# Kernel optimization log

Measured on AMD Instinct MI355X. Metric: run time of the kernel, lower is better.

Reference implementation:

```python
import jax, jax.numpy as jnp
import numpy as np

DIM_CODES = 512
DICT_SIZE = 512
EMBED_DIM = 16
BATCH = 512


def setup_inputs() -> dict:
    key = jax.random.key(0)
    k1, k2 = jax.random.split(key)
    mu = jax.random.normal(k1, (BATCH, DIM_CODES * EMBED_DIM), dtype=jnp.float32)
    dictionary = jax.random.normal(k2, (DIM_CODES, DICT_SIZE, EMBED_DIM), dtype=jnp.float32)
    return {"mu": mu, "dictionary": dictionary}


def reference(mu, dictionary):
    # mu: [B, C*E], dictionary: [C, K, E]
    B = mu.shape[0]
    C, K, E = dictionary.shape
    mu3 = mu.reshape(B, C, E)
    # pairwise squared distance ||mu - d||^2 = ||mu||^2 + ||d||^2 - 2 mu.d -> [B, C, K]
    dist = (jnp.sum(mu3 * mu3, axis=-1)[..., None]
            + jnp.sum(dictionary * dictionary, axis=-1)[None]
            - 2.0 * jnp.einsum('bce,cke->bck', mu3, dictionary))
    idx = jnp.argmin(dist, axis=-1)  # [B, C] int
    # gather nearest codebook entries: per-code index into its own codebook
    z_embed = dictionary[jnp.arange(C)[None, :], idx]  # [B, C, E]
    z_embed = z_embed.reshape(B, C * E)
    # TransferGrad: forward = z_embed, backward passes grad straight-through to mu
    z = mu + jax.lax.stop_gradient(z_embed - mu)
    one_hot_idx = jax.nn.one_hot(idx, K, dtype=mu.dtype)  # [B, C, K]
    return z, z_embed, one_hot_idx
```

## Files before the change

### kernel.cpp

```cpp
#include <hip/hip_runtime.h>
#include <float.h>

constexpr int C    = 512;
constexpr int K    = 512;
constexpr int E    = 16;
constexpr int B    = 512;
constexpr int ROWS = 128;
constexpr int MUS  = C * E;

__launch_bounds__(256, 2)
__global__ void vq_kernel(const float* __restrict__ mu,
                          const float* __restrict__ dict,
                          float* __restrict__ z,
                          float* __restrict__ zq,
                          float* __restrict__ oh)
{
    const int c    = blockIdx.x;
    const int b0   = blockIdx.y * ROWS;
    const int tid  = threadIdx.x;
    const int lane = tid & 63;
    const int wave = tid >> 6;

    __shared__ float mu_s[ROWS][E];

    const float* __restrict__ dbase = dict + (size_t)c * K * E;

    float4 dv[8][4];
    float  nrm[8];
#pragma unroll
    for (int i = 0; i < 8; ++i) {
        const int k = lane + 64 * i;
        const float4* p = reinterpret_cast<const float4*>(dbase + k * E);
        dv[i][0] = p[0]; dv[i][1] = p[1]; dv[i][2] = p[2]; dv[i][3] = p[3];
        float s = dv[i][0].x * dv[i][0].x;
        s = fmaf(dv[i][0].y, dv[i][0].y, s);
        s = fmaf(dv[i][0].z, dv[i][0].z, s);
        s = fmaf(dv[i][0].w, dv[i][0].w, s);
#pragma unroll
        for (int t = 1; t < 4; ++t) {
            s = fmaf(dv[i][t].x, dv[i][t].x, s);
            s = fmaf(dv[i][t].y, dv[i][t].y, s);
            s = fmaf(dv[i][t].z, dv[i][t].z, s);
            s = fmaf(dv[i][t].w, dv[i][t].w, s);
        }
        nrm[i] = s;
    }

    {
        const int r = tid >> 2, q = tid & 3;
#pragma unroll
        for (int rep = 0; rep < 2; ++rep) {
            const int row = r + rep * 64;
            const float4* p = reinterpret_cast<const float4*>(
                mu + (size_t)(b0 + row) * MUS + c * E);
            reinterpret_cast<float4*>(&mu_s[row][0])[q] = p[q];
        }
    }
    __syncthreads();

    auto compute_row = [&](int bl, float& obd, float& osec, int& obk) {
        float4 m[4];
#pragma unroll
        for (int t = 0; t < 4; ++t)
            m[t] = reinterpret_cast<const float4*>(&mu_s[bl][0])[t];

        float nm = m[0].x * m[0].x;
        nm = fmaf(m[0].y, m[0].y, nm);
        nm = fmaf(m[0].z, m[0].z, nm);
        nm = fmaf(m[0].w, m[0].w, nm);
#pragma unroll
        for (int t = 1; t < 4; ++t) {
            nm = fmaf(m[t].x, m[t].x, nm);
            nm = fmaf(m[t].y, m[t].y, nm);
            nm = fmaf(m[t].z, m[t].z, nm);
            nm = fmaf(m[t].w, m[t].w, nm);
        }

        float bdl = FLT_MAX, secl = FLT_MAX;
        int   bkl = K;
#pragma unroll
        for (int i = 0; i < 8; ++i) {
            float acc = dv[i][0].x * m[0].x;
            acc = fmaf(dv[i][0].y, m[0].y, acc);
            acc = fmaf(dv[i][0].z, m[0].z, acc);
            acc = fmaf(dv[i][0].w, m[0].w, acc);
#pragma unroll
            for (int t = 1; t < 4; ++t) {
                acc = fmaf(dv[i][t].x, m[t].x, acc);
                acc = fmaf(dv[i][t].y, m[t].y, acc);
                acc = fmaf(dv[i][t].z, m[t].z, acc);
                acc = fmaf(dv[i][t].w, m[t].w, acc);
            }
            const float dist = fmaf(-2.0f, acc, nm + nrm[i]);
            const int   k    = lane + 64 * i;
            const bool  lt   = dist < bdl;
            secl = lt ? bdl : fminf(secl, dist);
            bdl  = lt ? dist : bdl;
            bkl  = lt ? k : bkl;
        }
        obd = bdl; osec = secl; obk = bkl;
    };

    auto emit_row = [&](int bl_, float bd, float sec, int bk) {
        const int b = b0 + bl_;

        float w = bd;
#pragma unroll
        for (int off = 32; off; off >>= 1)
            w = fminf(w, __shfl_xor(w, off));

        const unsigned long long mask = __ballot(bd == w);
        const int lane0 = __ffsll(mask) - 1;
        int best_k = __shfl(bk, lane0);

        const float cand = (lane == lane0) ? sec : bd;
        if (__any(cand < w + 1e-3f)) {
            float mf[E];
#pragma unroll
            for (int t = 0; t < E; ++t) mf[t] = mu_s[bl_][t];
            double nmuD = 0.0;
#pragma unroll
            for (int t = 0; t < E; ++t) nmuD += (double)mf[t] * mf[t];

            double bD = DBL_MAX;
            int    bK = K;
#pragma unroll
            for (int i = 0; i < 8; ++i) {
                double nd = 0.0, dt = 0.0;
#pragma unroll
                for (int t = 0; t < 4; ++t) {
                    nd += (double)dv[i][t].x * dv[i][t].x
                        + (double)dv[i][t].y * dv[i][t].y
                        + (double)dv[i][t].z * dv[i][t].z
                        + (double)dv[i][t].w * dv[i][t].w;
                    dt += (double)dv[i][t].x * mf[4 * t + 0]
                        + (double)dv[i][t].y * mf[4 * t + 1]
                        + (double)dv[i][t].z * mf[4 * t + 2]
                        + (double)dv[i][t].w * mf[4 * t + 3];
                }
                const double dist = nmuD + nd - 2.0 * dt;
                const int k = lane + 64 * i;
                if (dist < bD) { bD = dist; bK = k; }
            }
#pragma unroll
            for (int off = 32; off; off >>= 1) {
                const double od = __shfl_down(bD, off);
                const int    ok = __shfl_down(bK, off);
                if (od < bD || (od == bD && ok < bK)) { bD = od; bK = ok; }
            }
            best_k = __shfl(bK, 0);
        }

        float* ohp = oh + ((size_t)b * C + c) * K;
#pragma unroll
        for (int h = 0; h < 2; ++h) {
            const int kb = h * 256 + lane * 4;
            float4 v;
            v.x = (kb + 0 == best_k) ? 1.0f : 0.0f;
            v.y = (kb + 1 == best_k) ? 1.0f : 0.0f;
            v.z = (kb + 2 == best_k) ? 1.0f : 0.0f;
            v.w = (kb + 3 == best_k) ? 1.0f : 0.0f;
            *reinterpret_cast<float4*>(ohp + kb) = v;
        }

        if (lane < E) {
            const float dq = dbase[best_k * E + lane];
            const float mm = mu_s[bl_][lane];
            const size_t o = (size_t)b * MUS + (size_t)c * E + lane;
            zq[o] = dq;
            z[o]  = mm + (dq - mm);
        }
    };

    {
        int   pbl = wave;
        float pbd, psec;
        int   pbk;
        compute_row(pbl, pbd, psec, pbk);

        for (int j = 1; j < ROWS / 4; ++j) {
            const int cbl = wave + 4 * j;
            float cbd, csec;
            int   cbk;
            compute_row(cbl, cbd, csec, cbk);
            emit_row(pbl, pbd, psec, pbk);
            pbl = cbl; pbd = cbd; psec = csec; pbk = cbk;
        }
        emit_row(pbl, pbd, psec, pbk);
    }
}

extern "C" void kernel_launch(void* const* d_in, const int* in_sizes, int n_in,
                              void* d_out, int out_size, void* d_ws, size_t ws_size,
                              hipStream_t stream)
{
    const float* mu   = (const float*)d_in[0];
    const float* dict = (const float*)d_in[1];

    float* z  = (float*)d_out;
    float* zq = z  + (size_t)B * C * E;
    float* oh = zq + (size_t)B * C * E;

    dim3 grid(C, B / ROWS);
    vq_kernel<<<grid, 256, 0, stream>>>(mu, dict, z, zq, oh);
}
```

Measured before the change: 751.1 us.

## Stage codebook in shared memory and assign one batch row per thread

```diff
diff --git a/kernel.cpp b/kernel.cpp
--- a/kernel.cpp
+++ b/kernel.cpp
@@ -5,10 +5,10 @@
 constexpr int K    = 512;
 constexpr int E    = 16;
 constexpr int B    = 512;
-constexpr int ROWS = 128;
+constexpr int RB   = 256;
 constexpr int MUS  = C * E;
 
-__launch_bounds__(256, 2)
+__launch_bounds__(256, 4)
 __global__ void vq_kernel(const float* __restrict__ mu,
                           const float* __restrict__ dict,
                           float* __restrict__ z,
@@ -16,177 +16,142 @@
                           float* __restrict__ oh)
 {
     const int c    = blockIdx.x;
-    const int b0   = blockIdx.y * ROWS;
+    const int b0   = blockIdx.y * RB;
     const int tid  = threadIdx.x;
     const int lane = tid & 63;
     const int wave = tid >> 6;
 
-    __shared__ float mu_s[ROWS][E];
+    __shared__ __align__(16) float dict_s[K * E];
+    __shared__ float nrm_s[K];
 
     const float* __restrict__ dbase = dict + (size_t)c * K * E;
 
-    float4 dv[8][4];
-    float  nrm[8];
 #pragma unroll
-    for (int i = 0; i < 8; ++i) {
-        const int k = lane + 64 * i;
+    for (int rep = 0; rep < 2; ++rep) {
+        const int k = tid + rep * 256;
         const float4* p = reinterpret_cast<const float4*>(dbase + k * E);
-        dv[i][0] = p[0]; dv[i][1] = p[1]; dv[i][2] = p[2]; dv[i][3] = p[3];
-        float s = dv[i][0].x * dv[i][0].x;
-        s = fmaf(dv[i][0].y, dv[i][0].y, s);
-        s = fmaf(dv[i][0].z, dv[i][0].z, s);
-        s = fmaf(dv[i][0].w, dv[i][0].w, s);
-#pragma unroll
-        for (int t = 1; t < 4; ++t) {
-            s = fmaf(dv[i][t].x, dv[i][t].x, s);
-            s = fmaf(dv[i][t].y, dv[i][t].y, s);
-            s = fmaf(dv[i][t].z, dv[i][t].z, s);
-            s = fmaf(dv[i][t].w, dv[i][t].w, s);
-        }
-        nrm[i] = s;
-    }
-
-    {
-        const int r = tid >> 2, q = tid & 3;
-#pragma unroll
-        for (int rep = 0; rep < 2; ++rep) {
-            const int row = r + rep * 64;
-            const float4* p = reinterpret_cast<const float4*>(
-                mu + (size_t)(b0 + row) * MUS + c * E);
-            reinterpret_cast<float4*>(&mu_s[row][0])[q] = p[q];
-        }
+        const float4 d0 = p[0], d1 = p[1], d2 = p[2], d3 = p[3];
+        float s = d0.x * d0.x;
+        s = fmaf(d0.y, d0.y, s); s = fmaf(d0.z, d0.z, s); s = fmaf(d0.w, d0.w, s);
+        s = fmaf(d1.x, d1.x, s); s = fmaf(d1.y, d1.y, s);
+        s = fmaf(d1.z, d1.z, s); s = fmaf(d1.w, d1.w, s);
+        s = fmaf(d2.x, d2.x, s); s = fmaf(d2.y, d2.y, s);
+        s = fmaf(d2.z, d2.z, s); s = fmaf(d2.w, d2.w, s);
+        s = fmaf(d3.x, d3.x, s); s = fmaf(d3.y, d3.y, s);
+        s = fmaf(d3.z, d3.z, s); s = fmaf(d3.w, d3.w, s);
+        float4* q4 = reinterpret_cast<float4*>(&dict_s[k * E]);
+        q4[0] = d0; q4[1] = d1; q4[2] = d2; q4[3] = d3;
+        nrm_s[k] = s;
     }
     __syncthreads();
 
-    auto compute_row = [&](int bl, float& obd, float& osec, int& obk) {
-        float4 m[4];
+    const int myrow = (wave << 6) + lane;
+    const float* __restrict__ mrow = mu + (size_t)(b0 + myrow) * MUS + c * E;
+    float4 m0, m1, m2, m3;
+    {
+        const float4* p = reinterpret_cast<const float4*>(mrow);
+        m0 = p[0]; m1 = p[1]; m2 = p[2]; m3 = p[3];
+    }
+    float nm = m0.x * m0.x;
+    nm = fmaf(m0.y, m0.y, nm); nm = fmaf(m0.z, m0.z, nm); nm = fmaf(m0.w, m0.w, nm);
+    nm = fmaf(m1.x, m1.x, nm); nm = fmaf(m1.y, m1.y, nm);
+    nm = fmaf(m1.z, m1.z, nm); nm = fmaf(m1.w, m1.w, nm);
+    nm = fmaf(m2.x, m2.x, nm); nm = fmaf(m2.y, m2.y, nm);
+    nm = fmaf(m2.z, m2.z, nm); nm = fmaf(m2.w, m2.w, nm);
+    nm = fmaf(m3.x, m3.x, nm); nm = fmaf(m3.y, m3.y, nm);
+    nm = fmaf(m3.z, m3.z, nm); nm = fmaf(m3.w, m3.w, nm);
+
+    float bd = FLT_MAX, sec = FLT_MAX;
+    int   bk = K;
+    const float4* __restrict__ ds4 = reinterpret_cast<const float4*>(dict_s);
+#pragma unroll 4
+    for (int k = 0; k < K; ++k) {
+        const float4 d0 = ds4[k * 4 + 0];
+        const float4 d1 = ds4[k * 4 + 1];
+        const float4 d2 = ds4[k * 4 + 2];
+        const float4 d3 = ds4[k * 4 + 3];
+        float acc = d0.x * m0.x;
+        acc = fmaf(d0.y, m0.y, acc); acc = fmaf(d0.z, m0.z, acc); acc = fmaf(d0.w, m0.w, acc);
+        acc = fmaf(d1.x, m1.x, acc); acc = fmaf(d1.y, m1.y, acc);
+        acc = fmaf(d1.z, m1.z, acc); acc = fmaf(d1.w, m1.w, acc);
+        acc = fmaf(d2.x, m2.x, acc); acc = fmaf(d2.y, m2.y, acc);
+        acc = fmaf(d2.z, m2.z, acc); acc = fmaf(d2.w, m2.w, acc);
+        acc = fmaf(d3.x, m3.x, acc); acc = fmaf(d3.y, m3.y, acc);
+        acc = fmaf(d3.z, m3.z, acc); acc = fmaf(d3.w, m3.w, acc);
+        const float dist = fmaf(-2.0f, acc, nm + nrm_s[k]);
+        const bool  lt   = dist < bd;
+        sec = lt ? bd : fminf(sec, dist);
+        bd  = lt ? dist : bd;
+        bk  = lt ? k : bk;
+    }
+
+    unsigned long long trig = __ballot(sec < bd + 1e-3f);
+    while (trig) {
+        const int r = __ffsll(trig) - 1;
+        trig &= trig - 1;
+        const int row = (wave << 6) + r;
+        const float* __restrict__ qrow = mu + (size_t)(b0 + row) * MUS + c * E;
+
+        double nmuD = 0.0;
 #pragma unroll
-        for (int t = 0; t < 4; ++t)
-            m[t] = reinterpret_cast<const float4*>(&mu_s[bl][0])[t];
-
-        float nm = m[0].x * m[0].x;
-        nm = fmaf(m[0].y, m[0].y, nm);
-        nm = fmaf(m[0].z, m[0].z, nm);
-        nm = fmaf(m[0].w, m[0].w, nm);
-#pragma unroll
-        for (int t = 1; t < 4; ++t) {
-            nm = fmaf(m[t].x, m[t].x, nm);
-            nm = fmaf(m[t].y, m[t].y, nm);
-            nm = fmaf(m[t].z, m[t].z, nm);
-            nm = fmaf(m[t].w, m[t].w, nm);
+        for (int t = 0; t < E; ++t) {
+            const double mt = (double)qrow[t];
+            nmuD += mt * mt;
         }
-
-        float bdl = FLT_MAX, secl = FLT_MAX;
-        int   bkl = K;
+        double bD = DBL_MAX;
+        int    bK = K;
 #pragma unroll
         for (int i = 0; i < 8; ++i) {
-            float acc = dv[i][0].x * m[0].x;
-            acc = fmaf(dv[i][0].y, m[0].y, acc);
-            acc = fmaf(dv[i][0].z, m[0].z, acc);
-            acc = fmaf(dv[i][0].w, m[0].w, acc);
+            const int k = lane + 64 * i;
+            const float* dk = &dict_s[k * E];
+            double nd = 0.0, dt = 0.0;
 #pragma unroll
-            for (int t = 1; t < 4; ++t) {
-                acc = fmaf(dv[i][t].x, m[t].x, acc);
-                acc = fmaf(dv[i][t].y, m[t].y, acc);
-                acc = fmaf(dv[i][t].z, m[t].z, acc);
-                acc = fmaf(dv[i][t].w, m[t].w, acc);
+            for (int t = 0; t < 4; ++t) {
+                const double dx = dk[4 * t + 0], dy = dk[4 * t + 1];
+                const double dz = dk[4 * t + 2], dw = dk[4 * t + 3];
+                const double mx = qrow[4 * t + 0], my = qrow[4 * t + 1];
+                const double mz = qrow[4 * t + 2], mw = qrow[4 * t + 3];
+                nd += dx * dx + dy * dy + dz * dz + dw * dw;
+                dt += dx * mx + dy * my + dz * mz + dw * mw;
             }
-            const float dist = fmaf(-2.0f, acc, nm + nrm[i]);
-            const int   k    = lane + 64 * i;
-            const bool  lt   = dist < bdl;
-            secl = lt ? bdl : fminf(secl, dist);
-            bdl  = lt ? dist : bdl;
-            bkl  = lt ? k : bkl;
+            const double dist = nmuD + nd - 2.0 * dt;
+            if (dist < bD) { bD = dist; bK = k; }
         }
-        obd = bdl; osec = secl; obk = bkl;
-    };
+#pragma unroll
+        for (int off = 32; off; off >>= 1) {
+            const double od = __shfl_down(bD, off);
+            const int    ok = __shfl_down(bK, off);
+            if (od < bD || (od == bD && ok < bK)) { bD = od; bK = ok; }
+        }
+        const int kwin = __shfl(bK, 0);
+        if (lane == r) bk = kwin;
+    }
 
-    auto emit_row = [&](int bl_, float bd, float sec, int bk) {
-        const int b = b0 + bl_;
-
-        float w = bd;
-#pragma unroll
-        for (int off = 32; off; off >>= 1)
-            w = fminf(w, __shfl_xor(w, off));
-
-        const unsigned long long mask = __ballot(bd == w);
-        const int lane0 = __ffsll(mask) - 1;
-        int best_k = __shfl(bk, lane0);
-
-        const float cand = (lane == lane0) ? sec : bd;
-        if (__any(cand < w + 1e-3f)) {
-            float mf[E];
-#pragma unroll
-            for (int t = 0; t < E; ++t) mf[t] = mu_s[bl_][t];
-            double nmuD = 0.0;
-#pragma unroll
-            for (int t = 0; t < E; ++t) nmuD += (double)mf[t] * mf[t];
-
-            double bD = DBL_MAX;
-            int    bK = K;
-#pragma unroll
-            for (int i = 0; i < 8; ++i) {
-                double nd = 0.0, dt = 0.0;
-#pragma unroll
-                for (int t = 0; t < 4; ++t) {
-                    nd += (double)dv[i][t].x * dv[i][t].x
-                        + (double)dv[i][t].y * dv[i][t].y
-                        + (double)dv[i][t].z * dv[i][t].z
-                        + (double)dv[i][t].w * dv[i][t].w;
-                    dt += (double)dv[i][t].x * mf[4 * t + 0]
-                        + (double)dv[i][t].y * mf[4 * t + 1]
-                        + (double)dv[i][t].z * mf[4 * t + 2]
-                        + (double)dv[i][t].w * mf[4 * t + 3];
-                }
-                const double dist = nmuD + nd - 2.0 * dt;
-                const int k = lane + 64 * i;
-                if (dist < bD) { bD = dist; bK = k; }
-            }
-#pragma unroll
-            for (int off = 32; off; off >>= 1) {
-                const double od = __shfl_down(bD, off);
-                const int    ok = __shfl_down(bK, off);
-                if (od < bD || (od == bD && ok < bK)) { bD = od; bK = ok; }
-            }
-            best_k = __shfl(bK, 0);
-        }
+#pragma unroll 4
+    for (int r = 0; r < 64; ++r) {
+        const int kk  = __shfl(bk, r);
+        const int row = (wave << 6) + r;
+        const int b   = b0 + row;
 
         float* ohp = oh + ((size_t)b * C + c) * K;
 #pragma unroll
         for (int h = 0; h < 2; ++h) {
             const int kb = h * 256 + lane * 4;
             float4 v;
-            v.x = (kb + 0 == best_k) ? 1.0f : 0.0f;
-            v.y = (kb + 1 == best_k) ? 1.0f : 0.0f;
-            v.z = (kb + 2 == best_k) ? 1.0f : 0.0f;
-            v.w = (kb + 3 == best_k) ? 1.0f : 0.0f;
+            v.x = (kb + 0 == kk) ? 1.0f : 0.0f;
+            v.y = (kb + 1 == kk) ? 1.0f : 0.0f;
+            v.z = (kb + 2 == kk) ? 1.0f : 0.0f;
+            v.w = (kb + 3 == kk) ? 1.0f : 0.0f;
             *reinterpret_cast<float4*>(ohp + kb) = v;
         }
 
         if (lane < E) {
-            const float dq = dbase[best_k * E + lane];
-            const float mm = mu_s[bl_][lane];
+            const float dq = dict_s[kk * E + lane];
+            const float mm = mu[(size_t)b * MUS + (size_t)c * E + lane];
             const size_t o = (size_t)b * MUS + (size_t)c * E + lane;
             zq[o] = dq;
             z[o]  = mm + (dq - mm);
         }
-    };
-
-    {
-        int   pbl = wave;
-        float pbd, psec;
-        int   pbk;
-        compute_row(pbl, pbd, psec, pbk);
-
-        for (int j = 1; j < ROWS / 4; ++j) {
-            const int cbl = wave + 4 * j;
-            float cbd, csec;
-            int   cbk;
-            compute_row(cbl, cbd, csec, cbk);
-            emit_row(pbl, pbd, psec, pbk);
-            pbl = cbl; pbd = cbd; psec = csec; pbk = cbk;
-        }
-        emit_row(pbl, pbd, psec, pbk);
     }
 }
 
@@ -201,6 +166,6 @@
     float* zq = z  + (size_t)B * C * E;
     float* oh = zq + (size_t)B * C * E;
 
-    dim3 grid(C, B / ROWS);
+    dim3 grid(C, B / RB);
     vq_kernel<<<grid, 256, 0, stream>>>(mu, dict, z, zq, oh);
 }
```

Measured after the change: 701.5 us. 1.07x faster.
